# Optimization experiments

Measured on AMD Instinct MI355X. Metric: run time of the kernel, lower is better.

## Reference

```python
import jax, jax.numpy as jnp
import numpy as np

EMB_DIM = 128
MID = 192  # ceil(1.5 * emb_dim)
VOCAB = 3000
KCLS = 5
B = 16
S = 128
EPS = 1e-5


def _linear_init(k, fin, fout):
    k1, k2 = jax.random.split(k)
    bound = 1.0 / np.sqrt(fin)
    W = jax.random.uniform(k1, (fin, fout), minval=-bound, maxval=bound, dtype=jnp.float32)
    b = jax.random.uniform(k2, (fout,), minval=-bound, maxval=bound, dtype=jnp.float32)
    return W, b


def setup_inputs() -> dict:
    key = jax.random.key(0)
    ks = jax.random.split(key, 7)
    emb = jax.random.normal(ks[0], (VOCAB, EMB_DIM), dtype=jnp.float32)
    W1, b1 = _linear_init(ks[1], 2 * EMB_DIM, MID)   # encoder layer 1
    W2, b2 = _linear_init(ks[2], MID, EMB_DIM)       # encoder layer 2
    W3, b3 = _linear_init(ks[3], EMB_DIM, MID)       # decoder layer 1
    W4, b4 = _linear_init(ks[4], MID, 2 * EMB_DIM)   # decoder layer 2
    Wk, bk = _linear_init(ks[5], EMB_DIM, KCLS)      # soft head
    inputs = jax.random.randint(ks[6], (B, S), 0, VOCAB, dtype=jnp.int64)
    return dict(inputs=inputs, emb=emb, W1=W1, b1=b1, W2=W2, b2=b2,
                W3=W3, b3=b3, W4=W4, b4=b4, Wk=Wk, bk=bk)


def _forward(inputs, emb, W1, b1, W2, b2, W3, b3, W4, b4, Wk, bk):
    X = emb[inputs]                      # (B,S,m)
    Bs, Sl, m = X.shape
    bidx = jnp.arange(Bs)
    karr = jnp.arange(Sl)
    jarr = jnp.arange(Sl - 1)

    def step(carry, t):
        nodes, counts, acc = carry       # (B,S,m), (B,S), (B,)
        L = Sl - t                       # current active list length
        right, left = nodes[:, 1:], nodes[:, :-1]          # pair j = (node[j+1], node[j])
        y = (jnp.concatenate([right, left], -1) @ W1 + b1) @ W2 + b2   # (B,S-1,m)
        xx = (y @ W3 + b3) @ W4 + b4                                    # (B,S-1,2m)
        # torch cross_entropy with float-vector target: -sum(target * log_softmax(input))
        ls1 = -(right * jax.nn.log_softmax(xx[..., :m], -1)).sum(-1)
        ls2 = -(left * jax.nn.log_softmax(xx[..., m:], -1)).sum(-1)
        n1, n2 = counts[:, 1:], counts[:, :-1]
        loss = ((n1 + EPS) * ls1 + (n2 + EPS) * ls2) / (n1 + n2 + EPS)
        valid = jarr < (L - 1)                                          # only first L-1 pairs active
        idx = jnp.argmin(jnp.where(valid[None, :], loss, jnp.inf), axis=1)  # (B,)
        acc = acc + jnp.take_along_axis(loss, idx[:, None], 1)[:, 0]
        father_x = jnp.take_along_axis(y, idx[:, None, None], 1)[:, 0]  # (B,m)
        # faithful bug: lc = nodelist[idx-1] (python wrap to L-1 when idx==0), rc = nodelist[idx]
        lc_idx = jnp.where(idx == 0, L - 1, idx - 1)
        father_cnt = (jnp.take_along_axis(counts, idx[:, None], 1)[:, 0]
                      + jnp.take_along_axis(counts, lc_idx[:, None], 1)[:, 0])
        pos = jnp.maximum(idx - 1, 0)
        # new list: drop lc and rc, father lands at pos; gather map reproduces list insert/remove
        src = jnp.where((idx[:, None] == 0) | (karr[None, :] < idx[:, None] - 1),
                        karr[None, :], karr[None, :] + 1)
        src = jnp.minimum(src, Sl - 1)
        nodes = jnp.take_along_axis(nodes, src[:, :, None], 1).at[bidx, pos].set(father_x)
        counts = jnp.take_along_axis(counts, src, 1).at[bidx, pos].set(father_cnt)
        return (nodes, counts, acc), None

    init = (X, jnp.ones((Bs, Sl), X.dtype), jnp.zeros((Bs,), X.dtype))
    (nodes, counts, acc), _ = jax.lax.scan(step, init, jnp.arange(Sl - 1))
    pred = jnp.argmax(nodes[:, 0] @ Wk + bk, axis=-1)   # argmax softmax == argmax logits
    return pred, acc.sum() / Bs


def reference(inputs, emb, W1, b1, W2, b2, W3, b3, W4, b4, Wk, bk):
    return _forward(inputs, emb, W1, b1, W2, b2, W3, b3, W4, b4, Wk, bk)
```

## Files before the change

### kernel.cpp

```cpp
#include <hip/hip_runtime.h>
#include <math.h>

#define EMB 128
#define MID 192
#define SEQ 128
#define BATCH 16
#define NPAIR 127
#define KCLS 5
#define EPSF 1e-5f

#define OFF_WYT   0
#define OFF_BY    32768
#define OFF_WXXT  32896
#define OFF_BXX   65664
#define OFF_NODES 65920
#define OFF_YC    328064
#define OFF_L0    588160

__global__ void k_comp(const float* __restrict__ W1, const float* __restrict__ b1,
                       const float* __restrict__ W2, const float* __restrict__ b2,
                       const float* __restrict__ W3, const float* __restrict__ b3,
                       const float* __restrict__ W4, const float* __restrict__ b4,
                       float* __restrict__ ws) {
    int tid = blockIdx.x * blockDim.x + threadIdx.x;
    if (tid < 32768) {
        int k = tid >> 7, o = tid & 127;
        float a = 0.f;
        for (int j = 0; j < MID; ++j) a += W1[k*MID+j] * W2[j*EMB+o];
        int q = k >> 6, jj = k & 63;
        ws[OFF_WYT + (size_t)(q*128 + o)*64 + jj] = a;
    } else if (tid < 65536) {
        int t = tid - 32768;
        int k = t >> 8, c = t & 255;
        float a = 0.f;
        for (int j = 0; j < MID; ++j) a += W3[k*MID+j] * W4[j*256+c];
        int hh = k >> 6, jj = k & 63;
        ws[OFF_WXXT + (size_t)(hh*256 + c)*64 + jj] = a;
    } else if (tid < 65536 + 128) {
        int o = tid - 65536;
        float a = b2[o];
        for (int j = 0; j < MID; ++j) a += b1[j] * W2[j*EMB+o];
        ws[OFF_BY + o] = a;
    } else if (tid < 65536 + 128 + 256) {
        int o = tid - 65536 - 128;
        float a = b4[o];
        for (int j = 0; j < MID; ++j) a += b3[j] * W4[j*256+o];
        ws[OFF_BXX + o] = a;
    }
}

__global__ void k_nodes(const int* __restrict__ inp, const float* __restrict__ emb,
                        float* __restrict__ ws) {
    int tid = blockIdx.x * blockDim.x + threadIdx.x;
    if (tid >= BATCH*SEQ*EMB) return;
    int d = tid & 127;
    int bs = tid >> 7;
    int tok = inp[bs];
    ws[OFF_NODES + tid] = emb[tok*EMB + d];
}

__global__ void __launch_bounds__(512, 2) k_init(float* __restrict__ ws) {
    __shared__ float s_x[2][2*EMB];
    __shared__ float s_red[4][2][EMB];
    __shared__ float s_redx[2][2][256];
    __shared__ float s_y[2][EMB];
    __shared__ float s_by[EMB];
    __shared__ float s_bxx[2*EMB];
    __shared__ float s_ls[2][2];
    int tid = threadIdx.x;
    int b = blockIdx.x >> 3, g = blockIdx.x & 7;
    float wy[64], wxx[64];
    {
        const float4* gw = (const float4*)(ws + OFF_WYT) + (size_t)tid*16;
        #pragma unroll
        for (int i = 0; i < 16; ++i) { float4 v = gw[i]; wy[4*i]=v.x; wy[4*i+1]=v.y; wy[4*i+2]=v.z; wy[4*i+3]=v.w; }
        const float4* gx = (const float4*)(ws + OFF_WXXT) + (size_t)tid*16;
        #pragma unroll
        for (int i = 0; i < 16; ++i) { float4 v = gx[i]; wxx[4*i]=v.x; wxx[4*i+1]=v.y; wxx[4*i+2]=v.z; wxx[4*i+3]=v.w; }
    }
    if (tid < EMB) s_by[tid] = ws[OFF_BY + tid];
    if (tid < 2*EMB) s_bxx[tid] = ws[OFF_BXX + tid];
    const float* nodes = ws + OFF_NODES + (size_t)b*SEQ*EMB;
    float* yc = ws + OFF_YC + (size_t)b*NPAIR*EMB;
    int q4 = tid >> 7, o = tid & 127;
    int hh = tid >> 8, c = tid & 255;
    int p_s = tid >> 8, kk = tid & 255;
    __syncthreads();
    for (int i = 0; i < 8; ++i) {
        int base = g*16 + i*2;
        {
            int j = base + p_s;
            int jj = j < NPAIR ? j : NPAIR - 1;
            s_x[p_s][kk] = nodes[(jj + (kk < 128 ? 1 : 0))*EMB + (kk & 127)];
        }
        __syncthreads();
        float a0 = 0.f, a1 = 0.f;
        #pragma unroll
        for (int j = 0; j < 64; ++j) {
            float w = wy[j];
            a0 += s_x[0][q4*64 + j] * w;
            a1 += s_x[1][q4*64 + j] * w;
        }
        s_red[q4][0][o] = a0;
        s_red[q4][1][o] = a1;
        __syncthreads();
        if (tid < 256) {
            int p = tid >> 7, oo = tid & 127;
            float yv = s_red[0][p][oo] + s_red[1][p][oo] + s_red[2][p][oo] + s_red[3][p][oo] + s_by[oo];
            s_y[p][oo] = yv;
            int j2 = base + p;
            if (j2 < NPAIR) yc[(size_t)j2*EMB + oo] = yv;
        }
        __syncthreads();
        float c0 = 0.f, c1 = 0.f;
        #pragma unroll
        for (int j = 0; j < 64; ++j) {
            float w = wxx[j];
            c0 += s_y[0][hh*64 + j] * w;
            c1 += s_y[1][hh*64 + j] * w;
        }
        s_redx[hh][0][c] = c0;
        s_redx[hh][1][c] = c1;
        __syncthreads();
        if (tid < 256) {
            int w = tid >> 6, lane = tid & 63;
            int p2 = w >> 1, h2 = w & 1;
            int cA = h2*128 + lane, cB = cA + 64;
            float v0 = s_redx[0][p2][cA] + s_redx[1][p2][cA] + s_bxx[cA];
            float v1 = s_redx[0][p2][cB] + s_redx[1][p2][cB] + s_bxx[cB];
            float m = fmaxf(v0, v1);
            for (int s = 32; s; s >>= 1) m = fmaxf(m, __shfl_xor(m, s, 64));
            float se = expf(v0 - m) + expf(v1 - m);
            for (int s = 32; s; s >>= 1) se += __shfl_xor(se, s, 64);
            float lse = m + logf(se);
            float o0 = s_x[p2][cA], o1 = s_x[p2][cB];
            float term = o0*(v0 - lse) + o1*(v1 - lse);
            for (int s = 32; s; s >>= 1) term += __shfl_xor(term, s, 64);
            if (lane == 0) s_ls[p2][h2] = -term;
        }
        __syncthreads();
        if (tid < 2) {
            int j2 = base + tid;
            if (j2 < NPAIR) {
                float l = ((1.f+EPSF)*s_ls[tid][0] + (1.f+EPSF)*s_ls[tid][1]) / (2.f + EPSF);
                ws[OFF_L0 + b*NPAIR + j2] = l;
            }
        }
        __syncthreads();
    }
}

__global__ void __launch_bounds__(512, 2) k_seq(float* __restrict__ ws,
                      const float* __restrict__ Wk, const float* __restrict__ bkv,
                      float* __restrict__ out) {
    __shared__ float s_nodes[SEQ*EMB];
    __shared__ float s_yc[NPAIR*EMB];
    __shared__ float s_x[2][2*EMB];
    __shared__ float s_red[4][2][EMB];
    __shared__ float s_redx[2][2][256];
    __shared__ float s_y[2][EMB];
    __shared__ float s_by[EMB];
    __shared__ float s_bxx[2*EMB];
    __shared__ float s_ls[2][2];
    __shared__ float s_loss[NPAIR];
    __shared__ float s_cnt[SEQ];
    __shared__ int   s_nslot[SEQ];
    __shared__ int   s_yslot[NPAIR];
    __shared__ int   s_q[2];
    __shared__ float s_wv[2];
    __shared__ int   s_wi[2];
    __shared__ float s_log[KCLS];

    int tid = threadIdx.x;
    int b = blockIdx.x;
    float wy[64], wxx[64];
    {
        const float4* gw = (const float4*)(ws + OFF_WYT) + (size_t)tid*16;
        #pragma unroll
        for (int i = 0; i < 16; ++i) { float4 v = gw[i]; wy[4*i]=v.x; wy[4*i+1]=v.y; wy[4*i+2]=v.z; wy[4*i+3]=v.w; }
        const float4* gx = (const float4*)(ws + OFF_WXXT) + (size_t)tid*16;
        #pragma unroll
        for (int i = 0; i < 16; ++i) { float4 v = gx[i]; wxx[4*i]=v.x; wxx[4*i+1]=v.y; wxx[4*i+2]=v.z; wxx[4*i+3]=v.w; }
    }
    {
        const float4* gn = (const float4*)(ws + OFF_NODES + (size_t)b*SEQ*EMB);
        float4* sn = (float4*)s_nodes;
        for (int i = tid; i < SEQ*EMB/4; i += 512) sn[i] = gn[i];
        const float4* gy = (const float4*)(ws + OFF_YC + (size_t)b*NPAIR*EMB);
        float4* sy = (float4*)s_yc;
        for (int i = tid; i < NPAIR*EMB/4; i += 512) sy[i] = gy[i];
    }
    if (tid < EMB) s_by[tid] = ws[OFF_BY + tid];
    if (tid < 2*EMB) s_bxx[tid] = ws[OFF_BXX + tid];
    if (tid < NPAIR) { s_loss[tid] = ws[OFF_L0 + b*NPAIR + tid]; s_yslot[tid] = tid; }
    if (tid < SEQ)   { s_cnt[tid] = 1.f; s_nslot[tid] = tid; }
    float acc = 0.f;
    int q4 = tid >> 7, o = tid & 127;
    int hh = tid >> 8, c = tid & 255;
    int p_s = tid >> 8, kk = tid & 255;
    __syncthreads();

    #pragma unroll 1
    for (int t = 0; t < NPAIR; ++t) {
        int L = SEQ - t;
        if (t > 0) {
            {
                int q = s_q[p_s];
                s_x[p_s][kk] = s_nodes[s_nslot[q + (kk < 128 ? 1 : 0)]*EMB + (kk & 127)];
            }
            __syncthreads();
            float a0 = 0.f, a1 = 0.f;
            #pragma unroll
            for (int j = 0; j < 64; ++j) {
                float w = wy[j];
                a0 += s_x[0][q4*64 + j] * w;
                a1 += s_x[1][q4*64 + j] * w;
            }
            s_red[q4][0][o] = a0;
            s_red[q4][1][o] = a1;
            __syncthreads();
            if (tid < 256) {
                int p = tid >> 7, oo = tid & 127;
                float yv = s_red[0][p][oo] + s_red[1][p][oo] + s_red[2][p][oo] + s_red[3][p][oo] + s_by[oo];
                s_y[p][oo] = yv;
                s_yc[(size_t)s_yslot[s_q[p]]*EMB + oo] = yv;
            }
            __syncthreads();
            float c0 = 0.f, c1 = 0.f;
            #pragma unroll
            for (int j = 0; j < 64; ++j) {
                float w = wxx[j];
                c0 += s_y[0][hh*64 + j] * w;
                c1 += s_y[1][hh*64 + j] * w;
            }
            s_redx[hh][0][c] = c0;
            s_redx[hh][1][c] = c1;
            __syncthreads();
            if (tid < 256) {
                int w = tid >> 6, lane = tid & 63;
                int p2 = w >> 1, h2 = w & 1;
                int cA = h2*128 + lane, cB = cA + 64;
                float v0 = s_redx[0][p2][cA] + s_redx[1][p2][cA] + s_bxx[cA];
                float v1 = s_redx[0][p2][cB] + s_redx[1][p2][cB] + s_bxx[cB];
                float m = fmaxf(v0, v1);
                for (int s = 32; s; s >>= 1) m = fmaxf(m, __shfl_xor(m, s, 64));
                float se = expf(v0 - m) + expf(v1 - m);
                for (int s = 32; s; s >>= 1) se += __shfl_xor(se, s, 64);
                float lse = m + logf(se);
                float o0 = s_x[p2][cA], o1 = s_x[p2][cB];
                float term = o0*(v0 - lse) + o1*(v1 - lse);
                for (int s = 32; s; s >>= 1) term += __shfl_xor(term, s, 64);
                if (lane == 0) s_ls[p2][h2] = -term;
            }
            __syncthreads();
            if (tid < 2) {
                int qq = s_q[tid];
                float n1 = s_cnt[qq+1], n2 = s_cnt[qq];
                s_loss[qq] = ((n1+EPSF)*s_ls[tid][0] + (n2+EPSF)*s_ls[tid][1]) / (n1+n2+EPSF);
            }
            __syncthreads();
        }
        if (tid < 128) {
            float v = (tid < L-1) ? s_loss[tid] : INFINITY;
            int ii = tid;
            for (int s = 32; s; s >>= 1) {
                float ov = __shfl_xor(v, s, 64);
                int   oi = __shfl_xor(ii, s, 64);
                if (ov < v || (ov == v && oi < ii)) { v = ov; ii = oi; }
            }
            if ((tid & 63) == 0) { s_wv[tid>>6] = v; s_wi[tid>>6] = ii; }
        }
        __syncthreads();
        float bv0 = s_wv[0], bv1 = s_wv[1];
        int idx = (s_wv[1] < s_wv[0]) ? s_wi[1] : s_wi[0];
        if (tid == 0) acc += fminf(bv0, bv1);
        int pos = idx > 0 ? idx - 1 : 0;
        int slotF = s_nslot[pos];
        int ysI   = s_yslot[idx];
        float fcnt = s_cnt[idx] + s_cnt[idx == 0 ? L-1 : idx-1];
        bool doShift = (idx > 0);
        bool shL = doShift && tid >= pos+1 && tid <= L-3;
        bool shC = doShift && tid >= pos+1 && tid <= L-2;
        float nl = 0.f, nc = 0.f; int nn = 0, ny = 0;
        if (shL) { nl = s_loss[tid+1]; ny = s_yslot[tid+1]; }
        if (shC) { nc = s_cnt[tid+1];  nn = s_nslot[tid+1]; }
        float fx = (tid < EMB) ? s_yc[(size_t)ysI*EMB + tid] : 0.f;
        __syncthreads();
        if (tid < EMB) s_nodes[slotF*EMB + tid] = fx;
        if (shL) { s_loss[tid] = nl; s_yslot[tid] = ny; }
        if (shC) { s_cnt[tid]  = nc; s_nslot[tid] = nn; }
        if (tid == 0) {
            s_cnt[pos] = fcnt;
            s_q[0] = (pos >= 1) ? pos - 1 : pos;
            s_q[1] = pos;
        }
        __syncthreads();
    }
    if (tid < KCLS) {
        int slot0 = s_nslot[0];
        float a = bkv[tid];
        for (int k = 0; k < EMB; ++k) a += s_nodes[slot0*EMB + k] * Wk[k*KCLS + tid];
        s_log[tid] = a;
    }
    __syncthreads();
    if (tid == 0) {
        int best = 0;
        for (int cc = 1; cc < KCLS; ++cc) if (s_log[cc] > s_log[best]) best = cc;
        out[b] = (float)best;
        atomicAdd(&out[BATCH], acc * (1.f/16.f));
    }
}

extern "C" void kernel_launch(void* const* d_in, const int* in_sizes, int n_in,
                              void* d_out, int out_size, void* d_ws, size_t ws_size,
                              hipStream_t stream) {
    const int*   inp = (const int*)d_in[0];
    const float* emb = (const float*)d_in[1];
    const float* W1  = (const float*)d_in[2];
    const float* b1  = (const float*)d_in[3];
    const float* W2  = (const float*)d_in[4];
    const float* b2  = (const float*)d_in[5];
    const float* W3  = (const float*)d_in[6];
    const float* b3  = (const float*)d_in[7];
    const float* W4  = (const float*)d_in[8];
    const float* b4  = (const float*)d_in[9];
    const float* Wk  = (const float*)d_in[10];
    const float* bk  = (const float*)d_in[11];
    float* out = (float*)d_out;
    float* ws  = (float*)d_ws;

    hipMemsetAsync(d_out, 0, (size_t)out_size * sizeof(float), stream);

    k_comp<<<(65920 + 255) / 256, 256, 0, stream>>>(W1, b1, W2, b2, W3, b3, W4, b4, ws);
    k_nodes<<<(BATCH*SEQ*EMB + 255) / 256, 256, 0, stream>>>(inp, emb, ws);
    k_init<<<BATCH * 8, 512, 0, stream>>>(ws);
    k_seq<<<BATCH, 512, 0, stream>>>(ws, Wk, bk, out);
}
```

Baseline: 550.9 us.

## Read node vectors directly from shared nodes, drop staging copy and a barrier

In the sequential kernel, the first matvec now reads the selected node rows straight from s_nodes through slot indices. This removes the s_x staging copy and the barrier that followed it. The per-pair loss update is folded into the argmin pass, which removes one more barrier per step. Weights are kept as float4 registers and shared reads use float4 vectors. k_init is split over twice as many blocks, each doing fewer pair iterations. The catch is that more shared-memory reads go through indirect slot lookups, which may cause bank conflicts.

After: 566.0 us. 1.03x slower.

```diff
diff --git a/kernel.cpp b/kernel.cpp
--- a/kernel.cpp
+++ b/kernel.cpp
@@ -68,15 +68,15 @@
     __shared__ float s_bxx[2*EMB];
     __shared__ float s_ls[2][2];
     int tid = threadIdx.x;
-    int b = blockIdx.x >> 3, g = blockIdx.x & 7;
-    float wy[64], wxx[64];
+    int b = blockIdx.x >> 4, g = blockIdx.x & 15;
+    float4 wy4[16], wxx4[16];
     {
         const float4* gw = (const float4*)(ws + OFF_WYT) + (size_t)tid*16;
         #pragma unroll
-        for (int i = 0; i < 16; ++i) { float4 v = gw[i]; wy[4*i]=v.x; wy[4*i+1]=v.y; wy[4*i+2]=v.z; wy[4*i+3]=v.w; }
+        for (int i = 0; i < 16; ++i) wy4[i] = gw[i];
         const float4* gx = (const float4*)(ws + OFF_WXXT) + (size_t)tid*16;
         #pragma unroll
-        for (int i = 0; i < 16; ++i) { float4 v = gx[i]; wxx[4*i]=v.x; wxx[4*i+1]=v.y; wxx[4*i+2]=v.z; wxx[4*i+3]=v.w; }
+        for (int i = 0; i < 16; ++i) wxx4[i] = gx[i];
     }
     if (tid < EMB) s_by[tid] = ws[OFF_BY + tid];
     if (tid < 2*EMB) s_bxx[tid] = ws[OFF_BXX + tid];
@@ -86,23 +86,28 @@
     int hh = tid >> 8, c = tid & 255;
     int p_s = tid >> 8, kk = tid & 255;
     __syncthreads();
-    for (int i = 0; i < 8; ++i) {
-        int base = g*16 + i*2;
+    for (int it = 0; it < 4; ++it) {
+        int base = g*8 + it*2;
         {
             int j = base + p_s;
             int jj = j < NPAIR ? j : NPAIR - 1;
             s_x[p_s][kk] = nodes[(jj + (kk < 128 ? 1 : 0))*EMB + (kk & 127)];
         }
         __syncthreads();
-        float a0 = 0.f, a1 = 0.f;
-        #pragma unroll
-        for (int j = 0; j < 64; ++j) {
-            float w = wy[j];
-            a0 += s_x[0][q4*64 + j] * w;
-            a1 += s_x[1][q4*64 + j] * w;
-        }
-        s_red[q4][0][o] = a0;
-        s_red[q4][1][o] = a1;
+        {
+            const float4* sx4 = (const float4*)s_x;
+            float a0 = 0.f, a1 = 0.f;
+            #pragma unroll
+            for (int i = 0; i < 16; ++i) {
+                float4 w = wy4[i];
+                float4 x0 = sx4[q4*16 + i];
+                float4 x1 = sx4[64 + q4*16 + i];
+                a0 += x0.x*w.x + x0.y*w.y + x0.z*w.z + x0.w*w.w;
+                a1 += x1.x*w.x + x1.y*w.y + x1.z*w.z + x1.w*w.w;
+            }
+            s_red[q4][0][o] = a0;
+            s_red[q4][1][o] = a1;
+        }
         __syncthreads();
         if (tid < 256) {
             int p = tid >> 7, oo = tid & 127;
@@ -112,15 +117,20 @@
             if (j2 < NPAIR) yc[(size_t)j2*EMB + oo] = yv;
         }
         __syncthreads();
-        float c0 = 0.f, c1 = 0.f;
-        #pragma unroll
-        for (int j = 0; j < 64; ++j) {
-            float w = wxx[j];
-            c0 += s_y[0][hh*64 + j] * w;
-            c1 += s_y[1][hh*64 + j] * w;
-        }
-        s_redx[hh][0][c] = c0;
-        s_redx[hh][1][c] = c1;
+        {
+            const float4* sy4 = (const float4*)s_y;
+            float c0 = 0.f, c1 = 0.f;
+            #pragma unroll
+            for (int i = 0; i < 16; ++i) {
+                float4 w = wxx4[i];
+                float4 y0 = sy4[hh*16 + i];
+                float4 y1 = sy4[32 + hh*16 + i];
+                c0 += y0.x*w.x + y0.y*w.y + y0.z*w.z + y0.w*w.w;
+                c1 += y1.x*w.x + y1.y*w.y + y1.z*w.z + y1.w*w.w;
+            }
+            s_redx[hh][0][c] = c0;
+            s_redx[hh][1][c] = c1;
+        }
         __syncthreads();
         if (tid < 256) {
             int w = tid >> 6, lane = tid & 63;
@@ -155,7 +165,6 @@
                       float* __restrict__ out) {
     __shared__ float s_nodes[SEQ*EMB];
     __shared__ float s_yc[NPAIR*EMB];
-    __shared__ float s_x[2][2*EMB];
     __shared__ float s_red[4][2][EMB];
     __shared__ float s_redx[2][2][256];
     __shared__ float s_y[2][EMB];
@@ -173,14 +182,14 @@
 
     int tid = threadIdx.x;
     int b = blockIdx.x;
-    float wy[64], wxx[64];
+    float4 wy4[16], wxx4[16];
     {
         const float4* gw = (const float4*)(ws + OFF_WYT) + (size_t)tid*16;
         #pragma unroll
-        for (int i = 0; i < 16; ++i) { float4 v = gw[i]; wy[4*i]=v.x; wy[4*i+1]=v.y; wy[4*i+2]=v.z; wy[4*i+3]=v.w; }
+        for (int i = 0; i < 16; ++i) wy4[i] = gw[i];
         const float4* gx = (const float4*)(ws + OFF_WXXT) + (size_t)tid*16;
         #pragma unroll
-        for (int i = 0; i < 16; ++i) { float4 v = gx[i]; wxx[4*i]=v.x; wxx[4*i+1]=v.y; wxx[4*i+2]=v.z; wxx[4*i+3]=v.w; }
+        for (int i = 0; i < 16; ++i) wxx4[i] = gx[i];
     }
     {
         const float4* gn = (const float4*)(ws + OFF_NODES + (size_t)b*SEQ*EMB);
@@ -197,7 +206,6 @@
     float acc = 0.f;
     int q4 = tid >> 7, o = tid & 127;
     int hh = tid >> 8, c = tid & 255;
-    int p_s = tid >> 8, kk = tid & 255;
     __syncthreads();
 
     #pragma unroll 1
@@ -205,19 +213,25 @@
         int L = SEQ - t;
         if (t > 0) {
             {
-                int q = s_q[p_s];
-                s_x[p_s][kk] = s_nodes[s_nslot[q + (kk < 128 ? 1 : 0)]*EMB + (kk & 127)];
-            }
-            __syncthreads();
-            float a0 = 0.f, a1 = 0.f;
-            #pragma unroll
-            for (int j = 0; j < 64; ++j) {
-                float w = wy[j];
-                a0 += s_x[0][q4*64 + j] * w;
-                a1 += s_x[1][q4*64 + j] * w;
-            }
-            s_red[q4][0][o] = a0;
-            s_red[q4][1][o] = a1;
+                int r = (q4 < 2) ? 1 : 0;
+                int half = q4 & 1;
+                int slot0 = s_nslot[s_q[0] + r];
+                int slot1 = s_nslot[s_q[1] + r];
+                const float4* n4 = (const float4*)s_nodes;
+                int base0 = slot0*32 + half*16;
+                int base1 = slot1*32 + half*16;
+                float a0 = 0.f, a1 = 0.f;
+                #pragma unroll
+                for (int i = 0; i < 16; ++i) {
+                    float4 w = wy4[i];
+                    float4 x0 = n4[base0 + i];
+                    float4 x1 = n4[base1 + i];
+                    a0 += x0.x*w.x + x0.y*w.y + x0.z*w.z + x0.w*w.w;
+                    a1 += x1.x*w.x + x1.y*w.y + x1.z*w.z + x1.w*w.w;
+                }
+                s_red[q4][0][o] = a0;
+                s_red[q4][1][o] = a1;
+            }
             __syncthreads();
             if (tid < 256) {
                 int p = tid >> 7, oo = tid & 127;
@@ -226,15 +240,20 @@
                 s_yc[(size_t)s_yslot[s_q[p]]*EMB + oo] = yv;
             }
             __syncthreads();
-            float c0 = 0.f, c1 = 0.f;
-            #pragma unroll
-            for (int j = 0; j < 64; ++j) {
-                float w = wxx[j];
-                c0 += s_y[0][hh*64 + j] * w;
-                c1 += s_y[1][hh*64 + j] * w;
-            }
-            s_redx[hh][0][c] = c0;
-            s_redx[hh][1][c] = c1;
+            {
+                const float4* sy4 = (const float4*)s_y;
+                float c0 = 0.f, c1 = 0.f;
+                #pragma unroll
+                for (int i = 0; i < 16; ++i) {
+                    float4 w = wxx4[i];
+                    float4 y0 = sy4[hh*16 + i];
+                    float4 y1 = sy4[32 + hh*16 + i];
+                    c0 += y0.x*w.x + y0.y*w.y + y0.z*w.z + y0.w*w.w;
+                    c1 += y1.x*w.x + y1.y*w.y + y1.z*w.z + y1.w*w.w;
+                }
+                s_redx[hh][0][c] = c0;
+                s_redx[hh][1][c] = c1;
+            }
             __syncthreads();
             if (tid < 256) {
                 int w = tid >> 6, lane = tid & 63;
@@ -247,21 +266,26 @@
                 float se = expf(v0 - m) + expf(v1 - m);
                 for (int s = 32; s; s >>= 1) se += __shfl_xor(se, s, 64);
                 float lse = m + logf(se);
-                float o0 = s_x[p2][cA], o1 = s_x[p2][cB];
+                int slot = s_nslot[s_q[p2] + (h2 == 0 ? 1 : 0)];
+                float o0 = s_nodes[slot*EMB + lane];
+                float o1 = s_nodes[slot*EMB + 64 + lane];
                 float term = o0*(v0 - lse) + o1*(v1 - lse);
                 for (int s = 32; s; s >>= 1) term += __shfl_xor(term, s, 64);
                 if (lane == 0) s_ls[p2][h2] = -term;
             }
             __syncthreads();
-            if (tid < 2) {
-                int qq = s_q[tid];
-                float n1 = s_cnt[qq+1], n2 = s_cnt[qq];
-                s_loss[qq] = ((n1+EPSF)*s_ls[tid][0] + (n2+EPSF)*s_ls[tid][1]) / (n1+n2+EPSF);
-            }
-            __syncthreads();
         }
         if (tid < 128) {
-            float v = (tid < L-1) ? s_loss[tid] : INFINITY;
+            float v = INFINITY;
+            if (tid < L-1) {
+                v = s_loss[tid];
+                if (t > 0 && (tid == s_q[0] || tid == s_q[1])) {
+                    int which = (tid == s_q[0]) ? 0 : 1;
+                    float n1 = s_cnt[tid+1], n2 = s_cnt[tid];
+                    v = ((n1+EPSF)*s_ls[which][0] + (n2+EPSF)*s_ls[which][1]) / (n1+n2+EPSF);
+                    s_loss[tid] = v;
+                }
+            }
             int ii = tid;
             for (int s = 32; s; s >>= 1) {
                 float ov = __shfl_xor(v, s, 64);
@@ -272,7 +296,7 @@
         }
         __syncthreads();
         float bv0 = s_wv[0], bv1 = s_wv[1];
-        int idx = (s_wv[1] < s_wv[0]) ? s_wi[1] : s_wi[0];
+        int idx = (bv1 < bv0) ? s_wi[1] : s_wi[0];
         if (tid == 0) acc += fminf(bv0, bv1);
         int pos = idx > 0 ? idx - 1 : 0;
         int slotF = s_nslot[pos];
@@ -333,6 +357,6 @@
 
     k_comp<<<(65920 + 255) / 256, 256, 0, stream>>>(W1, b1, W2, b2, W3, b3, W4, b4, ws);
     k_nodes<<<(BATCH*SEQ*EMB + 255) / 256, 256, 0, stream>>>(inp, emb, ws);
-    k_init<<<BATCH * 8, 512, 0, stream>>>(ws);
+    k_init<<<BATCH * 16, 512, 0, stream>>>(ws);
     k_seq<<<BATCH, 512, 0, stream>>>(ws, Wk, bk, out);
 }
```
